# Optimization experiments

Hardware: AMD Instinct MI355X
Metric: run time of the kernel (lower is better)

## Reference

```python
import jax, jax.numpy as jnp
import numpy as np

N = 100000   # nodes
E = 3200000  # edges (avg degree 32)
G = 512      # graphs in batch
IN = 128     # in_channels
H1, C1 = 8, 8  # conv1 heads, per-head channels
OUT = 64     # out_channels (conv2, 1 head)
NEG_SLOPE = 0.2


def setup_inputs() -> dict:
    key = jax.random.key(0)
    ks = jax.random.split(key, 12)
    s = 0.1
    return dict(
        x=jax.random.normal(ks[0], (N, IN), jnp.float32),
        edge_index=jax.random.randint(ks[1], (2, E), 0, N),
        batch=jnp.sort(jax.random.randint(ks[2], (N,), 0, G)),
        W1=jax.random.normal(ks[3], (IN, H1 * C1), jnp.float32) * s,
        att_src1=jax.random.normal(ks[4], (H1, C1), jnp.float32) * s,
        att_dst1=jax.random.normal(ks[5], (H1, C1), jnp.float32) * s,
        b1=jnp.zeros((H1 * C1,), jnp.float32),
        W2=jax.random.normal(ks[6], (H1 * C1, OUT), jnp.float32) * s,
        att_src2=jax.random.normal(ks[7], (1, OUT), jnp.float32) * s,
        att_dst2=jax.random.normal(ks[8], (1, OUT), jnp.float32) * s,
        b2=jnp.zeros((OUT,), jnp.float32),
        lw1=jax.random.normal(ks[9], (OUT, 128), jnp.float32) * s,
        lb1=jnp.zeros((128,), jnp.float32),
        lw2=jax.random.normal(ks[10], (128, 1), jnp.float32) * s,
        lb2=jnp.zeros((1,), jnp.float32),
    )


def gat_layer(x, src, dst, W, a_src, a_dst, bias, heads, outc):
    # PyG GATConv (eval mode): linear -> per-edge leaky_relu attention ->
    # segment softmax over incoming edges per dst -> weighted scatter-add.
    n = x.shape[0]
    h = (x @ W).reshape(n, heads, outc)                      # [N,H,C]
    a_s = jnp.einsum('nhc,hc->nh', h, a_src)                 # [N,H]
    a_d = jnp.einsum('nhc,hc->nh', h, a_dst)
    e = jax.nn.leaky_relu(a_s[src] + a_d[dst], NEG_SLOPE)    # [E',H]
    m = jax.ops.segment_max(e, dst, num_segments=n)
    m = jax.lax.stop_gradient(jnp.where(jnp.isfinite(m), m, 0.0))
    ex = jnp.exp(e - m[dst])
    denom = jax.ops.segment_sum(ex, dst, num_segments=n)
    alpha = ex / jnp.maximum(denom[dst], 1e-16)              # [E',H]
    out = jax.ops.segment_sum(h[src] * alpha[:, :, None], dst, num_segments=n)
    return out.reshape(n, heads * outc) + bias


def reference(x, W1, att_src1, att_dst1, b1, W2, att_src2, att_dst2, b2,
              lw1, lb1, lw2, lb2, edge_index, batch):
    n = x.shape[0]
    loops = jnp.arange(n)                                    # add_self_loops=True
    src = jnp.concatenate([edge_index[0], loops])
    dst = jnp.concatenate([edge_index[1], loops])
    h = jax.nn.elu(gat_layer(x, src, dst, W1, att_src1, att_dst1, b1, H1, C1))
    h = gat_layer(h, src, dst, W2, att_src2, att_dst2, b2, 1, OUT)  # [N,OUT]
    # global_mean_pool
    s = jax.ops.segment_sum(h, batch, num_segments=G)
    cnt = jax.ops.segment_sum(jnp.ones((n, 1), h.dtype), batch, num_segments=G)
    g = s / jnp.maximum(cnt, 1.0)                            # [G,OUT]
    g = jax.nn.elu(g @ lw1 + lb1)
    return g @ lw2 + lb2                                     # [G,1]
```

## Files before the change

kernel.cpp:

```cpp
#include <hip/hip_runtime.h>
#include <hip/hip_fp16.h>
#include <math.h>

#define NN   100000
#define EE   3200000
#define GG   512
#define INC  128
#define D1   64
#define OUTC 64
#define HID  128
#define NEG  0.2f

#define BINS 391
#define BCAP 9216

typedef __attribute__((ext_vector_type(2))) float v2f;

__global__ __launch_bounds__(256)
void k_bucket(const int* __restrict__ srcv, const int* __restrict__ dstv,
              int* __restrict__ cursor, int* __restrict__ bucket) {
    __shared__ int hcnt[BINS];
    __shared__ int hbase[BINS];
    int tid = threadIdx.x;
    for (int i = tid; i < BINS; i += 256) hcnt[i] = 0;
    __syncthreads();
    int e0 = blockIdx.x * 2048;
    int bn[8], rk[8], pk[8];
#pragma unroll
    for (int q = 0; q < 8; ++q) {
        int e = e0 + q * 256 + tid;
        if (e < EE) {
            int s = srcv[e], d = dstv[e];
            bn[q] = d >> 8;
            pk[q] = (s << 8) | (d & 255);
            rk[q] = atomicAdd(&hcnt[bn[q]], 1);
        } else bn[q] = -1;
    }
    __syncthreads();
    for (int i = tid; i < BINS; i += 256) {
        int c = hcnt[i];
        hbase[i] = c ? atomicAdd(&cursor[i], c) : 0;
    }
    __syncthreads();
#pragma unroll
    for (int q = 0; q < 8; ++q) {
        if (bn[q] >= 0) {
            int p = hbase[bn[q]] + rk[q];
            if (p < BCAP) bucket[bn[q] * BCAP + p] = pk[q];
        }
    }
}

__global__ __launch_bounds__(256)
void k_binCSR(const int* __restrict__ cursor, const int* __restrict__ bucket,
              int* __restrict__ col, int* __restrict__ rbeg, int* __restrict__ rend) {
    __shared__ int cnt[256];
    __shared__ int tmp[256];
    __shared__ int cur[256];
    int b = blockIdx.x, tid = threadIdx.x;
    cnt[tid] = 0;
    __syncthreads();
    int m = cursor[b]; if (m > BCAP) m = BCAP;
    const int* seg = bucket + b * BCAP;
    for (int i = tid; i < m; i += 256)
        atomicAdd(&cnt[seg[i] & 255], 1);
    __syncthreads();
    tmp[tid] = cnt[tid];
    __syncthreads();
    for (int off = 1; off < 256; off <<= 1) {
        int t = (tid >= off) ? tmp[tid - off] : 0;
        __syncthreads();
        tmp[tid] += t;
        __syncthreads();
    }
    int excl = tmp[tid] - cnt[tid];
    int n = b * 256 + tid;
    if (n < NN) {
        rbeg[n] = b * BCAP + excl;
        rend[n] = b * BCAP + excl + cnt[tid];
    }
    cur[tid] = excl;
    __syncthreads();
    for (int i = tid; i < m; i += 256) {
        int pkv = seg[i];
        int r = atomicAdd(&cur[pkv & 255], 1);
        col[b * BCAP + r] = pkv >> 8;
    }
}

__global__ __launch_bounds__(256)
void k_lin1(const float* __restrict__ x, const float* __restrict__ W1,
            const float* __restrict__ att_s, const float* __restrict__ att_d,
            unsigned int* __restrict__ h1, __half* __restrict__ a_s,
            float* __restrict__ a_d) {
    __shared__ float4 sW4[INC * 16];
    __shared__ float sx[16][INC + 4];
    __shared__ float sh[16][D1];
    __shared__ float satt[2 * D1];
    int tid = threadIdx.x;
    const float4* W4 = (const float4*)W1;
    for (int i = tid; i < INC * 16; i += 256) sW4[i] = W4[i];
    if (tid < 128) satt[tid] = (tid < 64) ? att_s[tid] : att_d[tid - 64];
    int node0 = blockIdx.x * 16;
    for (int i = tid; i < 16 * 32; i += 256) {
        int r = i >> 5, kk = i & 31;
        float4 v = ((const float4*)x)[(node0 + r) * 32 + kk];
        sx[r][kk * 4 + 0] = v.x; sx[r][kk * 4 + 1] = v.y;
        sx[r][kk * 4 + 2] = v.z; sx[r][kk * 4 + 3] = v.w;
    }
    __syncthreads();
    int r = tid >> 4, cg = tid & 15;
    float4 acc = {0.f, 0.f, 0.f, 0.f};
#pragma unroll 8
    for (int k = 0; k < INC; ++k) {
        float xv = sx[r][k];
        float4 wv = sW4[k * 16 + cg];
        acc.x = fmaf(xv, wv.x, acc.x);
        acc.y = fmaf(xv, wv.y, acc.y);
        acc.z = fmaf(xv, wv.z, acc.z);
        acc.w = fmaf(xv, wv.w, acc.w);
    }
    int p = __builtin_amdgcn_cvt_pk_fp8_f32(acc.x, acc.y, 0, false);
    p = __builtin_amdgcn_cvt_pk_fp8_f32(acc.z, acc.w, p, true);
    h1[(node0 + r) * 16 + cg] = (unsigned int)p;
    sh[r][cg * 4 + 0] = acc.x; sh[r][cg * 4 + 1] = acc.y;
    sh[r][cg * 4 + 2] = acc.z; sh[r][cg * 4 + 3] = acc.w;
    __syncthreads();
    if (tid < 128) {
        int rr = tid >> 3, hh = tid & 7;
        float as = 0.f, ad = 0.f;
#pragma unroll
        for (int j = 0; j < 8; ++j) {
            float v = sh[rr][hh * 8 + j];
            as = fmaf(v, satt[hh * 8 + j], as);
            ad = fmaf(v, satt[64 + hh * 8 + j], ad);
        }
        int nb = node0 + rr;
        a_s[nb * 8 + hh] = __float2half(as);
        a_d[nb * 8 + hh] = ad;
    }
}

__global__ __launch_bounds__(256, 8)
void k_gat_agg1(const int* __restrict__ rbeg, const int* __restrict__ rend,
                const int* __restrict__ col,
                const __half* __restrict__ a_s, const float* __restrict__ a_d,
                const unsigned int* __restrict__ h1, const float* __restrict__ b1,
                float* __restrict__ out) {
    int wv = threadIdx.x >> 6;
    int lane = threadIdx.x & 63;
    int half = lane >> 5;
    int d = blockIdx.x * 8 + wv * 2 + half;
    int gs = (lane >> 3) & 3;
    int l = lane & 7;
    int rb = rbeg[d], re = rend[d];
    float adh = a_d[d * 8 + l];
    const uint2* hp = (const uint2*)h1;
    uint2 rself = hp[d * 8 + l];
    float asself = __half2float(a_s[d * 8 + l]);
    float ac[8] = {0.f,0.f,0.f,0.f,0.f,0.f,0.f,0.f};
    float denom = 0.f;
    int e = rb + gs;
    int s[4];
#pragma unroll
    for (int q = 0; q < 4; ++q) s[q] = col[e + 4 * q];
    for (; e + 12 < re; ) {
        uint2 rr[4]; float asv[4]; int sn[4];
#pragma unroll
        for (int q = 0; q < 4; ++q) rr[q] = hp[s[q] * 8 + l];
#pragma unroll
        for (int q = 0; q < 4; ++q) asv[q] = __half2float(a_s[s[q] * 8 + l]);
        int en = e + 16;
#pragma unroll
        for (int q = 0; q < 4; ++q) sn[q] = col[en + 4 * q];
#pragma unroll
        for (int q = 0; q < 4; ++q) {
            float xx = asv[q] + adh;
            xx = xx >= 0.f ? xx : NEG * xx;
            float w = __expf(xx);
            denom += w;
            v2f f0 = __builtin_amdgcn_cvt_pk_f32_fp8((int)rr[q].x, false);
            v2f f1 = __builtin_amdgcn_cvt_pk_f32_fp8((int)rr[q].x, true);
            v2f f2 = __builtin_amdgcn_cvt_pk_f32_fp8((int)rr[q].y, false);
            v2f f3 = __builtin_amdgcn_cvt_pk_f32_fp8((int)rr[q].y, true);
            ac[0] = fmaf(f0.x, w, ac[0]); ac[1] = fmaf(f0.y, w, ac[1]);
            ac[2] = fmaf(f1.x, w, ac[2]); ac[3] = fmaf(f1.y, w, ac[3]);
            ac[4] = fmaf(f2.x, w, ac[4]); ac[5] = fmaf(f2.y, w, ac[5]);
            ac[6] = fmaf(f3.x, w, ac[6]); ac[7] = fmaf(f3.y, w, ac[7]);
        }
        e = en;
#pragma unroll
        for (int q = 0; q < 4; ++q) s[q] = sn[q];
    }
    for (; e < re; e += 4) {
        int s0 = col[e];
        uint2 r0 = hp[s0 * 8 + l];
        float x0 = __half2float(a_s[s0 * 8 + l]) + adh;
        x0 = x0 >= 0.f ? x0 : NEG * x0;
        float w0 = __expf(x0);
        denom += w0;
        v2f f0 = __builtin_amdgcn_cvt_pk_f32_fp8((int)r0.x, false);
        v2f f1 = __builtin_amdgcn_cvt_pk_f32_fp8((int)r0.x, true);
        v2f f2 = __builtin_amdgcn_cvt_pk_f32_fp8((int)r0.y, false);
        v2f f3 = __builtin_amdgcn_cvt_pk_f32_fp8((int)r0.y, true);
        ac[0] = fmaf(f0.x, w0, ac[0]); ac[1] = fmaf(f0.y, w0, ac[1]);
        ac[2] = fmaf(f1.x, w0, ac[2]); ac[3] = fmaf(f1.y, w0, ac[3]);
        ac[4] = fmaf(f2.x, w0, ac[4]); ac[5] = fmaf(f2.y, w0, ac[5]);
        ac[6] = fmaf(f3.x, w0, ac[6]); ac[7] = fmaf(f3.y, w0, ac[7]);
    }
    if (gs == 0) {
        float es = asself + adh;
        es = es >= 0.f ? es : NEG * es;
        float w = __expf(es);
        denom += w;
        v2f f0 = __builtin_amdgcn_cvt_pk_f32_fp8((int)rself.x, false);
        v2f f1 = __builtin_amdgcn_cvt_pk_f32_fp8((int)rself.x, true);
        v2f f2 = __builtin_amdgcn_cvt_pk_f32_fp8((int)rself.y, false);
        v2f f3 = __builtin_amdgcn_cvt_pk_f32_fp8((int)rself.y, true);
        ac[0] = fmaf(f0.x, w, ac[0]); ac[1] = fmaf(f0.y, w, ac[1]);
        ac[2] = fmaf(f1.x, w, ac[2]); ac[3] = fmaf(f1.y, w, ac[3]);
        ac[4] = fmaf(f2.x, w, ac[4]); ac[5] = fmaf(f2.y, w, ac[5]);
        ac[6] = fmaf(f3.x, w, ac[6]); ac[7] = fmaf(f3.y, w, ac[7]);
    }
#pragma unroll
    for (int i = 0; i < 8; ++i) {
        ac[i] += __shfl_xor(ac[i], 8, 64);
        ac[i] += __shfl_xor(ac[i], 16, 64);
    }
    denom += __shfl_xor(denom, 8, 64);
    denom += __shfl_xor(denom, 16, 64);
    if (gs == 0) {
        float inv = 1.0f / denom;
        float4 b0 = ((const float4*)b1)[l * 2];
        float4 b4 = ((const float4*)b1)[l * 2 + 1];
        float4 r0, r1;
        r0.x = fmaf(ac[0], inv, b0.x); r0.x = r0.x > 0.f ? r0.x : expm1f(r0.x);
        r0.y = fmaf(ac[1], inv, b0.y); r0.y = r0.y > 0.f ? r0.y : expm1f(r0.y);
        r0.z = fmaf(ac[2], inv, b0.z); r0.z = r0.z > 0.f ? r0.z : expm1f(r0.z);
        r0.w = fmaf(ac[3], inv, b0.w); r0.w = r0.w > 0.f ? r0.w : expm1f(r0.w);
        r1.x = fmaf(ac[4], inv, b4.x); r1.x = r1.x > 0.f ? r1.x : expm1f(r1.x);
        r1.y = fmaf(ac[5], inv, b4.y); r1.y = r1.y > 0.f ? r1.y : expm1f(r1.y);
        r1.z = fmaf(ac[6], inv, b4.z); r1.z = r1.z > 0.f ? r1.z : expm1f(r1.z);
        r1.w = fmaf(ac[7], inv, b4.w); r1.w = r1.w > 0.f ? r1.w : expm1f(r1.w);
        ((float4*)out)[d * 16 + l * 2]     = r0;
        ((float4*)out)[d * 16 + l * 2 + 1] = r1;
    }
}

__global__ __launch_bounds__(256)
void k_lin2(const float* __restrict__ hin, const float* __restrict__ W2,
            const float* __restrict__ att_s, const float* __restrict__ att_d,
            unsigned int* __restrict__ h2, float* __restrict__ a_s,
            float* __restrict__ a_d) {
    __shared__ float4 sW4[D1 * 16];
    __shared__ float sx[16][D1 + 4];
    __shared__ float satt[2 * OUTC];
    int tid = threadIdx.x;
    const float4* W4 = (const float4*)W2;
    for (int i = tid; i < D1 * 16; i += 256) sW4[i] = W4[i];
    if (tid < 128) satt[tid] = (tid < 64) ? att_s[tid] : att_d[tid - 64];
    int node0 = blockIdx.x * 16;
    for (int i = tid; i < 16 * 16; i += 256) {
        int r = i >> 4, kk = i & 15;
        float4 v = ((const float4*)hin)[(node0 + r) * 16 + kk];
        sx[r][kk * 4 + 0] = v.x; sx[r][kk * 4 + 1] = v.y;
        sx[r][kk * 4 + 2] = v.z; sx[r][kk * 4 + 3] = v.w;
    }
    __syncthreads();
    int r = tid >> 4, cg = tid & 15;
    float4 acc = {0.f, 0.f, 0.f, 0.f};
#pragma unroll 8
    for (int k = 0; k < D1; ++k) {
        float xv = sx[r][k];
        float4 wv = sW4[k * 16 + cg];
        acc.x = fmaf(xv, wv.x, acc.x);
        acc.y = fmaf(xv, wv.y, acc.y);
        acc.z = fmaf(xv, wv.z, acc.z);
        acc.w = fmaf(xv, wv.w, acc.w);
    }
    int n = node0 + r;
    int p = __builtin_amdgcn_cvt_pk_fp8_f32(acc.x, acc.y, 0, false);
    p = __builtin_amdgcn_cvt_pk_fp8_f32(acc.z, acc.w, p, true);
    h2[n * 16 + cg] = (unsigned int)p;
    float vs = acc.x * satt[cg * 4] + acc.y * satt[cg * 4 + 1]
             + acc.z * satt[cg * 4 + 2] + acc.w * satt[cg * 4 + 3];
    float vd = acc.x * satt[64 + cg * 4] + acc.y * satt[64 + cg * 4 + 1]
             + acc.z * satt[64 + cg * 4 + 2] + acc.w * satt[64 + cg * 4 + 3];
    for (int off = 1; off < 16; off <<= 1) {
        vs += __shfl_xor(vs, off, 64);
        vd += __shfl_xor(vd, off, 64);
    }
    if (cg == 0) { a_s[n] = vs; a_d[n] = vd; }
}

__global__ __launch_bounds__(256, 8)
void k_gat_agg2(const int* __restrict__ rbeg, const int* __restrict__ rend,
                const int* __restrict__ col,
                const float* __restrict__ a_s, const float* __restrict__ a_d,
                const unsigned int* __restrict__ h2, const float* __restrict__ b2,
                const int* __restrict__ batch,
                float* __restrict__ pool, float* __restrict__ cnt) {
    __shared__ float sv[8][64];
    __shared__ int sgi[8];
    int wv = threadIdx.x >> 6;
    int lane = threadIdx.x & 63;
    int half = lane >> 5;
    int idx = wv * 2 + half;
    int d = blockIdx.x * 8 + idx;
    int gs = (lane >> 3) & 3;
    int l = lane & 7;
    int rb = rbeg[d], re = rend[d];
    float ad = a_d[d];
    const uint2* hp = (const uint2*)h2;
    uint2 rself = hp[d * 8 + l];
    float asself = a_s[d];
    if (gs == 0 && l == 0) sgi[idx] = batch[d];
    float ac[8] = {0.f,0.f,0.f,0.f,0.f,0.f,0.f,0.f};
    float denom = 0.f;
    int e = rb + gs;
    int s[4];
#pragma unroll
    for (int q = 0; q < 4; ++q) s[q] = col[e + 4 * q];
    for (; e + 12 < re; ) {
        uint2 rr[4]; float asv[4]; int sn[4];
#pragma unroll
        for (int q = 0; q < 4; ++q) rr[q] = hp[s[q] * 8 + l];
#pragma unroll
        for (int q = 0; q < 4; ++q) asv[q] = a_s[s[q]];
        int en = e + 16;
#pragma unroll
        for (int q = 0; q < 4; ++q) sn[q] = col[en + 4 * q];
#pragma unroll
        for (int q = 0; q < 4; ++q) {
            float xx = asv[q] + ad;
            xx = xx >= 0.f ? xx : NEG * xx;
            float w = __expf(xx);
            denom += w;
            v2f f0 = __builtin_amdgcn_cvt_pk_f32_fp8((int)rr[q].x, false);
            v2f f1 = __builtin_amdgcn_cvt_pk_f32_fp8((int)rr[q].x, true);
            v2f f2 = __builtin_amdgcn_cvt_pk_f32_fp8((int)rr[q].y, false);
            v2f f3 = __builtin_amdgcn_cvt_pk_f32_fp8((int)rr[q].y, true);
            ac[0] = fmaf(f0.x, w, ac[0]); ac[1] = fmaf(f0.y, w, ac[1]);
            ac[2] = fmaf(f1.x, w, ac[2]); ac[3] = fmaf(f1.y, w, ac[3]);
            ac[4] = fmaf(f2.x, w, ac[4]); ac[5] = fmaf(f2.y, w, ac[5]);
            ac[6] = fmaf(f3.x, w, ac[6]); ac[7] = fmaf(f3.y, w, ac[7]);
        }
        e = en;
#pragma unroll
        for (int q = 0; q < 4; ++q) s[q] = sn[q];
    }
    for (; e < re; e += 4) {
        int s0 = col[e];
        uint2 r0 = hp[s0 * 8 + l];
        float x0 = a_s[s0] + ad;
        x0 = x0 >= 0.f ? x0 : NEG * x0;
        float w0 = __expf(x0);
        denom += w0;
        v2f f0 = __builtin_amdgcn_cvt_pk_f32_fp8((int)r0.x, false);
        v2f f1 = __builtin_amdgcn_cvt_pk_f32_fp8((int)r0.x, true);
        v2f f2 = __builtin_amdgcn_cvt_pk_f32_fp8((int)r0.y, false);
        v2f f3 = __builtin_amdgcn_cvt_pk_f32_fp8((int)r0.y, true);
        ac[0] = fmaf(f0.x, w0, ac[0]); ac[1] = fmaf(f0.y, w0, ac[1]);
        ac[2] = fmaf(f1.x, w0, ac[2]); ac[3] = fmaf(f1.y, w0, ac[3]);
        ac[4] = fmaf(f2.x, w0, ac[4]); ac[5] = fmaf(f2.y, w0, ac[5]);
        ac[6] = fmaf(f3.x, w0, ac[6]); ac[7] = fmaf(f3.y, w0, ac[7]);
    }
    if (gs == 0) {
        float es = asself + ad;
        es = es >= 0.f ? es : NEG * es;
        float w = __expf(es);
        denom += w;
        v2f f0 = __builtin_amdgcn_cvt_pk_f32_fp8((int)rself.x, false);
        v2f f1 = __builtin_amdgcn_cvt_pk_f32_fp8((int)rself.x, true);
        v2f f2 = __builtin_amdgcn_cvt_pk_f32_fp8((int)rself.y, false);
        v2f f3 = __builtin_amdgcn_cvt_pk_f32_fp8((int)rself.y, true);
        ac[0] = fmaf(f0.x, w, ac[0]); ac[1] = fmaf(f0.y, w, ac[1]);
        ac[2] = fmaf(f1.x, w, ac[2]); ac[3] = fmaf(f1.y, w, ac[3]);
        ac[4] = fmaf(f2.x, w, ac[4]); ac[5] = fmaf(f2.y, w, ac[5]);
        ac[6] = fmaf(f3.x, w, ac[6]); ac[7] = fmaf(f3.y, w, ac[7]);
    }
#pragma unroll
    for (int i = 0; i < 8; ++i) {
        ac[i] += __shfl_xor(ac[i], 8, 64);
        ac[i] += __shfl_xor(ac[i], 16, 64);
    }
    denom += __shfl_xor(denom, 8, 64);
    denom += __shfl_xor(denom, 16, 64);
    if (gs == 0) {
        float inv = 1.0f / denom;
#pragma unroll
        for (int i = 0; i < 8; ++i)
            sv[idx][l * 8 + i] = fmaf(ac[i], inv, b2[l * 8 + i]);
    }
    __syncthreads();
    int tid = threadIdx.x;
    if (tid < 64) {
        float acc = sv[0][tid]; int curg = sgi[0];
        for (int r = 1; r < 8; ++r) {
            if (sgi[r] == curg) acc += sv[r][tid];
            else { atomicAdd(&pool[curg * 64 + tid], acc); curg = sgi[r]; acc = sv[r][tid]; }
        }
        atomicAdd(&pool[curg * 64 + tid], acc);
    } else if (tid == 64) {
        float c = 1.f; int curg = sgi[0];
        for (int r = 1; r < 8; ++r) {
            if (sgi[r] == curg) c += 1.f;
            else { atomicAdd(&cnt[curg], c); curg = sgi[r]; c = 1.f; }
        }
        atomicAdd(&cnt[curg], c);
    }
}

__global__ __launch_bounds__(128)
void k_mlp(const float* __restrict__ pool, const float* __restrict__ cnt,
           const float* __restrict__ lw1, const float* __restrict__ lb1,
           const float* __restrict__ lw2, const float* __restrict__ lb2,
           float* __restrict__ out) {
    __shared__ float sg[OUTC];
    __shared__ float sh[HID];
    int g = blockIdx.x, tid = threadIdx.x;
    float c = fmaxf(cnt[g], 1.0f);
    if (tid < OUTC) sg[tid] = pool[g * OUTC + tid] / c;
    __syncthreads();
    float acc = lb1[tid];
#pragma unroll 8
    for (int k = 0; k < OUTC; ++k)
        acc = fmaf(sg[k], lw1[k * HID + tid], acc);
    acc = acc > 0.f ? acc : expm1f(acc);
    sh[tid] = acc * lw2[tid];
    __syncthreads();
    for (int off = 64; off >= 1; off >>= 1) {
        if (tid < off) sh[tid] += sh[tid + off];
        __syncthreads();
    }
    if (tid == 0) out[g] = sh[0] + lb2[0];
}

extern "C" void kernel_launch(void* const* d_in, const int* in_sizes, int n_in,
                              void* d_out, int out_size, void* d_ws, size_t ws_size,
                              hipStream_t stream) {
    const float* x    = (const float*)d_in[0];
    const int*   ei   = (const int*)d_in[1];
    const int*   batch= (const int*)d_in[2];
    const float* W1   = (const float*)d_in[3];
    const float* as1  = (const float*)d_in[4];
    const float* ad1  = (const float*)d_in[5];
    const float* b1   = (const float*)d_in[6];
    const float* W2   = (const float*)d_in[7];
    const float* as2  = (const float*)d_in[8];
    const float* ad2  = (const float*)d_in[9];
    const float* b2   = (const float*)d_in[10];
    const float* lw1  = (const float*)d_in[11];
    const float* lb1  = (const float*)d_in[12];
    const float* lw2  = (const float*)d_in[13];
    const float* lb2  = (const float*)d_in[14];
    float* out = (float*)d_out;

    unsigned int* H8 = (unsigned int*)d_ws;
    float* B    = (float*)(H8 + (size_t)NN * 16);
    float* aD1  = B + (size_t)NN * 64;
    float* aS2  = aD1 + NN * 8;
    float* aD2  = aS2 + NN;
    float* pool = aD2 + NN;
    float* cnt  = pool + GG * 64;
    __half* aS1h = (__half*)(cnt + GG);
    int* rbeg   = (int*)(aS1h + (size_t)NN * 8);
    int* rend   = rbeg + NN;
    int* cursor = rend + NN;
    int* bucket = cursor + BINS;
    int* colv   = bucket + (size_t)BINS * BCAP;

    const int* srcv = ei;
    const int* dstv = ei + EE;

    hipMemsetAsync(cursor, 0, BINS * sizeof(int), stream);
    hipMemsetAsync(pool, 0, (size_t)(GG * 64 + GG) * sizeof(float), stream);

    k_bucket<<<(EE + 2047) / 2048, 256, 0, stream>>>(srcv, dstv, cursor, bucket);
    k_binCSR<<<BINS, 256, 0, stream>>>(cursor, bucket, colv, rbeg, rend);

    k_lin1    <<<NN / 16, 256, 0, stream>>>(x, W1, as1, ad1, H8, aS1h, aD1);
    k_gat_agg1<<<NN / 8, 256, 0, stream>>>(rbeg, rend, colv, aS1h, aD1, H8, b1, B);

    k_lin2    <<<NN / 16, 256, 0, stream>>>(B, W2, as2, ad2, H8, aS2, aD2);
    k_gat_agg2<<<NN / 8, 256, 0, stream>>>(rbeg, rend, colv, aS2, aD2, H8, b2, batch, pool, cnt);

    k_mlp<<<GG, 128, 0, stream>>>(pool, cnt, lw1, lb1, lw2, lb2, out);
}
```

Before: 402.5 us.

## Split node features into two half-tables and run aggregation per half

The fp8 feature table and the half-precision source attention scores are each split into two separate arrays, one per half of the channels. The aggregation kernels now launch twice as many blocks. Each block gathers only one half, so each lane walks 8 edge streams instead of 4, and an extra shuffle step does the reduction. The CSR bins are halved to 128 destinations each, and col loads and hidden stores use nontemporal hints. The aim is to shrink the random-gather working set per pass so it fits better in cache. The cost is reading the edge list twice and doubling the pool atomics.

```diff
diff --git a/kernel.cpp b/kernel.cpp
--- a/kernel.cpp
+++ b/kernel.cpp
@@ -11,18 +11,19 @@
 #define HID  128
 #define NEG  0.2f
 
-#define BINS 391
-#define BCAP 9216
+#define BINS2 782
+#define BCAP2 4864
 
 typedef __attribute__((ext_vector_type(2))) float v2f;
+typedef __attribute__((ext_vector_type(4))) float v4f;
 
 __global__ __launch_bounds__(256)
 void k_bucket(const int* __restrict__ srcv, const int* __restrict__ dstv,
               int* __restrict__ cursor, int* __restrict__ bucket) {
-    __shared__ int hcnt[BINS];
-    __shared__ int hbase[BINS];
+    __shared__ int hcnt[BINS2];
+    __shared__ int hbase[BINS2];
     int tid = threadIdx.x;
-    for (int i = tid; i < BINS; i += 256) hcnt[i] = 0;
+    for (int i = tid; i < BINS2; i += 256) hcnt[i] = 0;
     __syncthreads();
     int e0 = blockIdx.x * 2048;
     int bn[8], rk[8], pk[8];
@@ -31,13 +32,13 @@
         int e = e0 + q * 256 + tid;
         if (e < EE) {
             int s = srcv[e], d = dstv[e];
-            bn[q] = d >> 8;
-            pk[q] = (s << 8) | (d & 255);
+            bn[q] = d >> 7;
+            pk[q] = (s << 7) | (d & 127);
             rk[q] = atomicAdd(&hcnt[bn[q]], 1);
         } else bn[q] = -1;
     }
     __syncthreads();
-    for (int i = tid; i < BINS; i += 256) {
+    for (int i = tid; i < BINS2; i += 256) {
         int c = hcnt[i];
         hbase[i] = c ? atomicAdd(&cursor[i], c) : 0;
     }
@@ -46,7 +47,7 @@
     for (int q = 0; q < 8; ++q) {
         if (bn[q] >= 0) {
             int p = hbase[bn[q]] + rk[q];
-            if (p < BCAP) bucket[bn[q] * BCAP + p] = pk[q];
+            if (p < BCAP2) bucket[bn[q] * BCAP2 + p] = pk[q];
         }
     }
 }
@@ -54,18 +55,19 @@
 __global__ __launch_bounds__(256)
 void k_binCSR(const int* __restrict__ cursor, const int* __restrict__ bucket,
               int* __restrict__ col, int* __restrict__ rbeg, int* __restrict__ rend) {
-    __shared__ int cnt[256];
+    __shared__ int cnt[128];
     __shared__ int tmp[256];
-    __shared__ int cur[256];
+    __shared__ int cur[128];
     int b = blockIdx.x, tid = threadIdx.x;
-    cnt[tid] = 0;
-    __syncthreads();
-    int m = cursor[b]; if (m > BCAP) m = BCAP;
-    const int* seg = bucket + b * BCAP;
+    if (tid < 128) cnt[tid] = 0;
+    __syncthreads();
+    int m = cursor[b]; if (m > BCAP2) m = BCAP2;
+    const int* seg = bucket + b * BCAP2;
     for (int i = tid; i < m; i += 256)
-        atomicAdd(&cnt[seg[i] & 255], 1);
-    __syncthreads();
-    tmp[tid] = cnt[tid];
+        atomicAdd(&cnt[seg[i] & 127], 1);
+    __syncthreads();
+    int v = (tid < 128) ? cnt[tid] : 0;
+    tmp[tid] = v;
     __syncthreads();
     for (int off = 1; off < 256; off <<= 1) {
         int t = (tid >= off) ? tmp[tid - off] : 0;
@@ -73,25 +75,28 @@
         tmp[tid] += t;
         __syncthreads();
     }
-    int excl = tmp[tid] - cnt[tid];
-    int n = b * 256 + tid;
-    if (n < NN) {
-        rbeg[n] = b * BCAP + excl;
-        rend[n] = b * BCAP + excl + cnt[tid];
-    }
-    cur[tid] = excl;
+    if (tid < 128) {
+        int excl = tmp[tid] - v;
+        int n = b * 128 + tid;
+        if (n < NN) {
+            rbeg[n] = b * BCAP2 + excl;
+            rend[n] = b * BCAP2 + excl + v;
+        }
+        cur[tid] = excl;
+    }
     __syncthreads();
     for (int i = tid; i < m; i += 256) {
         int pkv = seg[i];
-        int r = atomicAdd(&cur[pkv & 255], 1);
-        col[b * BCAP + r] = pkv >> 8;
+        int r = atomicAdd(&cur[pkv & 127], 1);
+        col[b * BCAP2 + r] = pkv >> 7;
     }
 }
 
 __global__ __launch_bounds__(256)
 void k_lin1(const float* __restrict__ x, const float* __restrict__ W1,
             const float* __restrict__ att_s, const float* __restrict__ att_d,
-            unsigned int* __restrict__ h1, __half* __restrict__ a_s,
+            unsigned int* __restrict__ Ha, unsigned int* __restrict__ Hb,
+            __half* __restrict__ aSa, __half* __restrict__ aSb,
             float* __restrict__ a_d) {
     __shared__ float4 sW4[INC * 16];
     __shared__ float sx[16][INC + 4];
@@ -122,7 +127,8 @@
     }
     int p = __builtin_amdgcn_cvt_pk_fp8_f32(acc.x, acc.y, 0, false);
     p = __builtin_amdgcn_cvt_pk_fp8_f32(acc.z, acc.w, p, true);
-    h1[(node0 + r) * 16 + cg] = (unsigned int)p;
+    unsigned int* Ht = (cg < 8) ? Ha : Hb;
+    Ht[(node0 + r) * 8 + (cg & 7)] = (unsigned int)p;
     sh[r][cg * 4 + 0] = acc.x; sh[r][cg * 4 + 1] = acc.y;
     sh[r][cg * 4 + 2] = acc.z; sh[r][cg * 4 + 3] = acc.w;
     __syncthreads();
@@ -136,7 +142,8 @@
             ad = fmaf(v, satt[64 + hh * 8 + j], ad);
         }
         int nb = node0 + rr;
-        a_s[nb * 8 + hh] = __float2half(as);
+        __half* aSt = (hh < 4) ? aSa : aSb;
+        aSt[nb * 4 + (hh & 3)] = __float2half(as);
         a_d[nb * 8 + hh] = ad;
     }
 }
@@ -144,35 +151,41 @@
 __global__ __launch_bounds__(256, 8)
 void k_gat_agg1(const int* __restrict__ rbeg, const int* __restrict__ rend,
                 const int* __restrict__ col,
-                const __half* __restrict__ a_s, const float* __restrict__ a_d,
-                const unsigned int* __restrict__ h1, const float* __restrict__ b1,
-                float* __restrict__ out) {
+                const __half* __restrict__ aSa, const __half* __restrict__ aSb,
+                const float* __restrict__ a_d,
+                const unsigned int* __restrict__ Ha, const unsigned int* __restrict__ Hb,
+                const float* __restrict__ b1, float* __restrict__ out) {
+    int bid = blockIdx.x;
+    int ng   = (bid >> 3) * 4 + (bid & 3);
+    int half = (bid >> 2) & 1;
     int wv = threadIdx.x >> 6;
     int lane = threadIdx.x & 63;
-    int half = lane >> 5;
-    int d = blockIdx.x * 8 + wv * 2 + half;
-    int gs = (lane >> 3) & 3;
-    int l = lane & 7;
+    int hn = lane >> 5;
+    int d = ng * 8 + wv * 2 + hn;
+    int gs = (lane >> 2) & 7;
+    int l = lane & 3;
+    int hd = half * 4 + l;
+    const uint2* hp = (const uint2*)(half ? Hb : Ha);
+    const __half* asp = half ? aSb : aSa;
     int rb = rbeg[d], re = rend[d];
-    float adh = a_d[d * 8 + l];
-    const uint2* hp = (const uint2*)h1;
-    uint2 rself = hp[d * 8 + l];
-    float asself = __half2float(a_s[d * 8 + l]);
+    float adh = a_d[d * 8 + hd];
+    uint2 rself = hp[d * 4 + l];
+    float asself = __half2float(asp[d * 4 + l]);
     float ac[8] = {0.f,0.f,0.f,0.f,0.f,0.f,0.f,0.f};
     float denom = 0.f;
     int e = rb + gs;
     int s[4];
 #pragma unroll
-    for (int q = 0; q < 4; ++q) s[q] = col[e + 4 * q];
-    for (; e + 12 < re; ) {
+    for (int q = 0; q < 4; ++q) s[q] = __builtin_nontemporal_load(col + e + 8 * q);
+    for (; e + 24 < re; ) {
         uint2 rr[4]; float asv[4]; int sn[4];
 #pragma unroll
-        for (int q = 0; q < 4; ++q) rr[q] = hp[s[q] * 8 + l];
-#pragma unroll
-        for (int q = 0; q < 4; ++q) asv[q] = __half2float(a_s[s[q] * 8 + l]);
-        int en = e + 16;
-#pragma unroll
-        for (int q = 0; q < 4; ++q) sn[q] = col[en + 4 * q];
+        for (int q = 0; q < 4; ++q) rr[q] = hp[s[q] * 4 + l];
+#pragma unroll
+        for (int q = 0; q < 4; ++q) asv[q] = __half2float(asp[s[q] * 4 + l]);
+        int en = e + 32;
+#pragma unroll
+        for (int q = 0; q < 4; ++q) sn[q] = __builtin_nontemporal_load(col + en + 8 * q);
 #pragma unroll
         for (int q = 0; q < 4; ++q) {
             float xx = asv[q] + adh;
@@ -192,10 +205,10 @@
 #pragma unroll
         for (int q = 0; q < 4; ++q) s[q] = sn[q];
     }
-    for (; e < re; e += 4) {
-        int s0 = col[e];
-        uint2 r0 = hp[s0 * 8 + l];
-        float x0 = __half2float(a_s[s0 * 8 + l]) + adh;
+    for (; e < re; e += 8) {
+        int s0 = __builtin_nontemporal_load(col + e);
+        uint2 r0 = hp[s0 * 4 + l];
+        float x0 = __half2float(asp[s0 * 4 + l]) + adh;
         x0 = x0 >= 0.f ? x0 : NEG * x0;
         float w0 = __expf(x0);
         denom += w0;
@@ -224,16 +237,18 @@
     }
 #pragma unroll
     for (int i = 0; i < 8; ++i) {
+        ac[i] += __shfl_xor(ac[i], 4, 64);
         ac[i] += __shfl_xor(ac[i], 8, 64);
         ac[i] += __shfl_xor(ac[i], 16, 64);
     }
+    denom += __shfl_xor(denom, 4, 64);
     denom += __shfl_xor(denom, 8, 64);
     denom += __shfl_xor(denom, 16, 64);
     if (gs == 0) {
         float inv = 1.0f / denom;
-        float4 b0 = ((const float4*)b1)[l * 2];
-        float4 b4 = ((const float4*)b1)[l * 2 + 1];
-        float4 r0, r1;
+        float4 b0 = ((const float4*)b1)[hd * 2];
+        float4 b4 = ((const float4*)b1)[hd * 2 + 1];
+        v4f r0, r1;
         r0.x = fmaf(ac[0], inv, b0.x); r0.x = r0.x > 0.f ? r0.x : expm1f(r0.x);
         r0.y = fmaf(ac[1], inv, b0.y); r0.y = r0.y > 0.f ? r0.y : expm1f(r0.y);
         r0.z = fmaf(ac[2], inv, b0.z); r0.z = r0.z > 0.f ? r0.z : expm1f(r0.z);
@@ -242,16 +257,16 @@
         r1.y = fmaf(ac[5], inv, b4.y); r1.y = r1.y > 0.f ? r1.y : expm1f(r1.y);
         r1.z = fmaf(ac[6], inv, b4.z); r1.z = r1.z > 0.f ? r1.z : expm1f(r1.z);
         r1.w = fmaf(ac[7], inv, b4.w); r1.w = r1.w > 0.f ? r1.w : expm1f(r1.w);
-        ((float4*)out)[d * 16 + l * 2]     = r0;
-        ((float4*)out)[d * 16 + l * 2 + 1] = r1;
+        __builtin_nontemporal_store(r0, (v4f*)out + d * 16 + hd * 2);
+        __builtin_nontemporal_store(r1, (v4f*)out + d * 16 + hd * 2 + 1);
     }
 }
 
 __global__ __launch_bounds__(256)
 void k_lin2(const float* __restrict__ hin, const float* __restrict__ W2,
             const float* __restrict__ att_s, const float* __restrict__ att_d,
-            unsigned int* __restrict__ h2, float* __restrict__ a_s,
-            float* __restrict__ a_d) {
+            unsigned int* __restrict__ Ha, unsigned int* __restrict__ Hb,
+            float* __restrict__ a_s, float* __restrict__ a_d) {
     __shared__ float4 sW4[D1 * 16];
     __shared__ float sx[16][D1 + 4];
     __shared__ float satt[2 * OUTC];
@@ -281,7 +296,8 @@
     int n = node0 + r;
     int p = __builtin_amdgcn_cvt_pk_fp8_f32(acc.x, acc.y, 0, false);
     p = __builtin_amdgcn_cvt_pk_fp8_f32(acc.z, acc.w, p, true);
-    h2[n * 16 + cg] = (unsigned int)p;
+    unsigned int* Ht = (cg < 8) ? Ha : Hb;
+    Ht[n * 8 + (cg & 7)] = (unsigned int)p;
     float vs = acc.x * satt[cg * 4] + acc.y * satt[cg * 4 + 1]
              + acc.z * satt[cg * 4 + 2] + acc.w * satt[cg * 4 + 3];
     float vd = acc.x * satt[64 + cg * 4] + acc.y * satt[64 + cg * 4 + 1]
@@ -297,22 +313,25 @@
 void k_gat_agg2(const int* __restrict__ rbeg, const int* __restrict__ rend,
                 const int* __restrict__ col,
                 const float* __restrict__ a_s, const float* __restrict__ a_d,
-                const unsigned int* __restrict__ h2, const float* __restrict__ b2,
-                const int* __restrict__ batch,
+                const unsigned int* __restrict__ Ha, const unsigned int* __restrict__ Hb,
+                const float* __restrict__ b2, const int* __restrict__ batch,
                 float* __restrict__ pool, float* __restrict__ cnt) {
-    __shared__ float sv[8][64];
+    __shared__ float sv[8][32];
     __shared__ int sgi[8];
+    int bid = blockIdx.x;
+    int ng   = (bid >> 3) * 4 + (bid & 3);
+    int half = (bid >> 2) & 1;
     int wv = threadIdx.x >> 6;
     int lane = threadIdx.x & 63;
-    int half = lane >> 5;
-    int idx = wv * 2 + half;
-    int d = blockIdx.x * 8 + idx;
-    int gs = (lane >> 3) & 3;
-    int l = lane & 7;
+    int hn = lane >> 5;
+    int idx = wv * 2 + hn;
+    int d = ng * 8 + idx;
+    int gs = (lane >> 2) & 7;
+    int l = lane & 3;
+    const uint2* hp = (const uint2*)(half ? Hb : Ha);
     int rb = rbeg[d], re = rend[d];
     float ad = a_d[d];
-    const uint2* hp = (const uint2*)h2;
-    uint2 rself = hp[d * 8 + l];
+    uint2 rself = hp[d * 4 + l];
     float asself = a_s[d];
     if (gs == 0 && l == 0) sgi[idx] = batch[d];
     float ac[8] = {0.f,0.f,0.f,0.f,0.f,0.f,0.f,0.f};
@@ -320,16 +339,16 @@
     int e = rb + gs;
     int s[4];
 #pragma unroll
-    for (int q = 0; q < 4; ++q) s[q] = col[e + 4 * q];
-    for (; e + 12 < re; ) {
+    for (int q = 0; q < 4; ++q) s[q] = __builtin_nontemporal_load(col + e + 8 * q);
+    for (; e + 24 < re; ) {
         uint2 rr[4]; float asv[4]; int sn[4];
 #pragma unroll
-        for (int q = 0; q < 4; ++q) rr[q] = hp[s[q] * 8 + l];
+        for (int q = 0; q < 4; ++q) rr[q] = hp[s[q] * 4 + l];
 #pragma unroll
         for (int q = 0; q < 4; ++q) asv[q] = a_s[s[q]];
-        int en = e + 16;
-#pragma unroll
-        for (int q = 0; q < 4; ++q) sn[q] = col[en + 4 * q];
+        int en = e + 32;
+#pragma unroll
+        for (int q = 0; q < 4; ++q) sn[q] = __builtin_nontemporal_load(col + en + 8 * q);
 #pragma unroll
         for (int q = 0; q < 4; ++q) {
             float xx = asv[q] + ad;
@@ -349,9 +368,9 @@
 #pragma unroll
         for (int q = 0; q < 4; ++q) s[q] = sn[q];
     }
-    for (; e < re; e += 4) {
-        int s0 = col[e];
-        uint2 r0 = hp[s0 * 8 + l];
+    for (; e < re; e += 8) {
+        int s0 = __builtin_nontemporal_load(col + e);
+        uint2 r0 = hp[s0 * 4 + l];
         float x0 = a_s[s0] + ad;
         x0 = x0 >= 0.f ? x0 : NEG * x0;
         float w0 = __expf(x0);
@@ -381,27 +400,29 @@
     }
 #pragma unroll
     for (int i = 0; i < 8; ++i) {
+        ac[i] += __shfl_xor(ac[i], 4, 64);
         ac[i] += __shfl_xor(ac[i], 8, 64);
         ac[i] += __shfl_xor(ac[i], 16, 64);
     }
+    denom += __shfl_xor(denom, 4, 64);
     denom += __shfl_xor(denom, 8, 64);
     denom += __shfl_xor(denom, 16, 64);
     if (gs == 0) {
         float inv = 1.0f / denom;
 #pragma unroll
         for (int i = 0; i < 8; ++i)
-            sv[idx][l * 8 + i] = fmaf(ac[i], inv, b2[l * 8 + i]);
+            sv[idx][l * 8 + i] = fmaf(ac[i], inv, b2[half * 32 + l * 8 + i]);
     }
     __syncthreads();
     int tid = threadIdx.x;
-    if (tid < 64) {
+    if (tid < 32) {
         float acc = sv[0][tid]; int curg = sgi[0];
         for (int r = 1; r < 8; ++r) {
             if (sgi[r] == curg) acc += sv[r][tid];
-            else { atomicAdd(&pool[curg * 64 + tid], acc); curg = sgi[r]; acc = sv[r][tid]; }
-        }
-        atomicAdd(&pool[curg * 64 + tid], acc);
-    } else if (tid == 64) {
+            else { atomicAdd(&pool[curg * 64 + half * 32 + tid], acc); curg = sgi[r]; acc = sv[r][tid]; }
+        }
+        atomicAdd(&pool[curg * 64 + half * 32 + tid], acc);
+    } else if (tid == 32 && half == 0) {
         float c = 1.f; int curg = sgi[0];
         for (int r = 1; r < 8; ++r) {
             if (sgi[r] == curg) c += 1.f;
@@ -456,34 +477,36 @@
     const float* lb2  = (const float*)d_in[14];
     float* out = (float*)d_out;
 
-    unsigned int* H8 = (unsigned int*)d_ws;
-    float* B    = (float*)(H8 + (size_t)NN * 16);
+    unsigned int* Ha = (unsigned int*)d_ws;
+    unsigned int* Hb = Ha + (size_t)NN * 8;
+    float* B    = (float*)(Hb + (size_t)NN * 8);
     float* aD1  = B + (size_t)NN * 64;
     float* aS2  = aD1 + NN * 8;
     float* aD2  = aS2 + NN;
     float* pool = aD2 + NN;
     float* cnt  = pool + GG * 64;
-    __half* aS1h = (__half*)(cnt + GG);
-    int* rbeg   = (int*)(aS1h + (size_t)NN * 8);
+    __half* aSa = (__half*)(cnt + GG);
+    __half* aSb = aSa + (size_t)NN * 4;
+    int* rbeg   = (int*)(aSb + (size_t)NN * 4);
     int* rend   = rbeg + NN;
     int* cursor = rend + NN;
-    int* bucket = cursor + BINS;
-    int* colv   = bucket + (size_t)BINS * BCAP;
+    int* bucket = cursor + BINS2;
+    int* colv   = bucket + (size_t)BINS2 * BCAP2;
 
     const int* srcv = ei;
     const int* dstv = ei + EE;
 
-    hipMemsetAsync(cursor, 0, BINS * sizeof(int), stream);
+    hipMemsetAsync(cursor, 0, BINS2 * sizeof(int), stream);
     hipMemsetAsync(pool, 0, (size_t)(GG * 64 + GG) * sizeof(float), stream);
 
     k_bucket<<<(EE + 2047) / 2048, 256, 0, stream>>>(srcv, dstv, cursor, bucket);
-    k_binCSR<<<BINS, 256, 0, stream>>>(cursor, bucket, colv, rbeg, rend);
-
-    k_lin1    <<<NN / 16, 256, 0, stream>>>(x, W1, as1, ad1, H8, aS1h, aD1);
-    k_gat_agg1<<<NN / 8, 256, 0, stream>>>(rbeg, rend, colv, aS1h, aD1, H8, b1, B);
-
-    k_lin2    <<<NN / 16, 256, 0, stream>>>(B, W2, as2, ad2, H8, aS2, aD2);
-    k_gat_agg2<<<NN / 8, 256, 0, stream>>>(rbeg, rend, colv, aS2, aD2, H8, b2, batch, pool, cnt);
+    k_binCSR<<<BINS2, 256, 0, stream>>>(cursor, bucket, colv, rbeg, rend);
+
+    k_lin1    <<<NN / 16, 256, 0, stream>>>(x, W1, as1, ad1, Ha, Hb, aSa, aSb, aD1);
+    k_gat_agg1<<<NN / 4, 256, 0, stream>>>(rbeg, rend, colv, aSa, aSb, aD1, Ha, Hb, b1, B);
+
+    k_lin2    <<<NN / 16, 256, 0, stream>>>(B, W2, as2, ad2, Ha, Hb, aS2, aD2);
+    k_gat_agg2<<<NN / 4, 256, 0, stream>>>(rbeg, rend, colv, aS2, aD2, Ha, Hb, b2, batch, pool, cnt);
 
     k_mlp<<<GG, 128, 0, stream>>>(pool, cnt, lw1, lb1, lw2, lb2, out);
 }
```

After: 508.6 us. +26.3%, slower.
